# Performance work log

Measured on AMD Instinct MI355X. Metric: run time of the kernel, lower is better.

The kernel has to match this reference:

```python
import jax, jax.numpy as jnp
import numpy as np

H = 256

def setup_inputs() -> dict:
    key = jax.random.key(0)
    ks = jax.random.split(key, 9)
    s = 1.0 / np.sqrt(H)
    x = jax.random.normal(ks[0], (8, 2048, H), dtype=jnp.float32)
    Wq = jax.random.uniform(ks[1], (H, H), jnp.float32, -s, s)
    bq = jax.random.uniform(ks[2], (H,), jnp.float32, -s, s)
    Wk = jax.random.uniform(ks[3], (H, H), jnp.float32, -s, s)
    bk = jax.random.uniform(ks[4], (H,), jnp.float32, -s, s)
    Wv = jax.random.uniform(ks[5], (H, H), jnp.float32, -s, s)
    bv = jax.random.uniform(ks[6], (H,), jnp.float32, -s, s)
    Ww = jax.random.uniform(ks[7], (H, 1), jnp.float32, -s, s)
    bw = jax.random.uniform(ks[8], (1,), jnp.float32, -s, s)
    return {"x": x, "Wq": Wq, "bq": bq, "Wk": Wk, "bk": bk,
            "Wv": Wv, "bv": bv, "Ww": Ww, "bw": bw}

def reference(x, Wq, bq, Wk, bk, Wv, bv, Ww, bw):
    # x: (B, N, H) — cross-asset attention over N assets
    q = x @ Wq + bq
    k = x @ Wk + bk
    v = x @ Wv + bv
    scale = 1.0 / jnp.sqrt(jnp.asarray(q.shape[-1], q.dtype))
    beta = jnp.einsum('bnd,bmd->bnm', q, k) * scale  # (B, N, N)
    beta = jax.nn.softmax(beta, axis=-1)
    # original: sum(value[:,None] * beta[...,None], dim=2) == beta @ v
    out = jnp.einsum('bnm,bmd->bnd', beta, v)
    final_scores = (out @ Ww + bw)[..., 0]  # (B, N)
    return final_scores
```

## Files before the change

### kernel.cpp

```cpp
#include <hip/hip_runtime.h>

#define H 256
#define NB 2048
#define BATCH 8
#define NSPLIT 8
#define KSPAN (NB / NSPLIT)
#define NITER (KSPAN / 64)

typedef unsigned short u16;
using bf16x8 = __attribute__((ext_vector_type(8))) __bf16;
using f32x4  = __attribute__((ext_vector_type(4))) float;

typedef const __attribute__((address_space(1))) void gv_t;
typedef __attribute__((address_space(3))) void lv_t;

__device__ __forceinline__ void gl_lds16(const void* g, void* l) {
    __builtin_amdgcn_global_load_lds((gv_t*)g, (lv_t*)l, 16, 0, 0);
}

#define MFMA(a, b, c) __builtin_amdgcn_mfma_f32_16x16x32_bf16(a, b, c, 0, 0, 0)

__device__ __forceinline__ u16 f2bf(float f) {
    union { float f; unsigned u; } v; v.f = f;
    unsigned r = v.u + 0x7fffu + ((v.u >> 16) & 1u);
    return (u16)(r >> 16);
}

__global__ __launch_bounds__(256) void wprep_kernel(
        const float* __restrict__ Wq, const float* __restrict__ Wk,
        const float* __restrict__ Wv, const float* __restrict__ Ww,
        const float* __restrict__ bq,
        u16* __restrict__ wqb, u16* __restrict__ wkb,
        float* __restrict__ wvw, float* __restrict__ kbv) {
    int f = blockIdx.x, t = threadIdx.x;
    float wq = Wq[f * H + t];
    wqb[f * H + t] = f2bf(wq);
    float wk = Wk[f * H + t];
    wkb[f * H + t] = f2bf(wk);
    float p = Wv[f * H + t] * Ww[t];
    float r = wk * bq[t];
    for (int o = 32; o; o >>= 1) { p += __shfl_xor(p, o); r += __shfl_xor(r, o); }
    __shared__ float redp[4], redr[4];
    int w = t >> 6, lane = t & 63;
    if (lane == 0) { redp[w] = p; redr[w] = r; }
    __syncthreads();
    if (t == 0) {
        wvw[f] = redp[0] + redp[1] + redp[2] + redp[3];
        kbv[f] = redr[0] + redr[1] + redr[2] + redr[3];
    }
}

__global__ __launch_bounds__(256) void cvtu_kernel(
        const float* __restrict__ x, const float* __restrict__ wvw,
        const float* __restrict__ kbv, const float* __restrict__ bv,
        const float* __restrict__ Ww,
        u16* __restrict__ xbf, float2* __restrict__ uee) {
    int lane = threadIdx.x & 63;
    int row  = blockIdx.x * 4 + (threadIdx.x >> 6);
    float4 xv = *(const float4*)(x + row * H + lane * 4);
    ushort4 o;
    o.x = f2bf(xv.x); o.y = f2bf(xv.y); o.z = f2bf(xv.z); o.w = f2bf(xv.w);
    *(ushort4*)(xbf + row * H + lane * 4) = o;
    float4 wv = *(const float4*)(wvw + lane * 4);
    float s = xv.x * wv.x + xv.y * wv.y + xv.z * wv.z + xv.w * wv.w;
    float4 kv = *(const float4*)(kbv + lane * 4);
    float d = xv.x * kv.x + xv.y * kv.y + xv.z * kv.z + xv.w * kv.w;
    float4 bvv = *(const float4*)(bv + lane * 4);
    float4 www = *(const float4*)(Ww + lane * 4);
    float c = bvv.x * www.x + bvv.y * www.y + bvv.z * www.z + bvv.w * www.w;
    for (int o2 = 32; o2; o2 >>= 1) {
        s += __shfl_xor(s, o2); d += __shfl_xor(d, o2); c += __shfl_xor(c, o2);
    }
    if (lane == 0) {
        float e = __expf(d * 0.0625f);
        uee[row] = make_float2(e * (s + c), e);
    }
}

__global__ __launch_bounds__(256) void gemm_bt_kernel(
        const u16* __restrict__ A, const u16* __restrict__ B,
        u16* __restrict__ C, float scale) {
    __shared__ u16 bt[16384];
    int tid = threadIdx.x;
    int mb = blockIdx.x * 128, nb = blockIdx.y * 64;
    int w = tid >> 6, lane = tid & 63;
    int l15 = lane & 15, quad = lane >> 4;

    {
        const u16* gsrc = B + (nb + w * 16 + l15) * H + quad * 8;
        for (int ks = 0; ks < 8; ++ks)
            gl_lds16(gsrc + ks * 32, bt + (w * 8 + ks) * 512);
    }

    bf16x8 a[2][8];
    for (int mi = 0; mi < 2; ++mi) {
        const u16* abase = A + (size_t)(mb + w * 32 + mi * 16 + l15) * H + quad * 8;
        for (int ks = 0; ks < 8; ++ks) a[mi][ks] = *(const bf16x8*)(abase + ks * 32);
    }
    __syncthreads();

    f32x4 acc[2][4] = {};
    for (int ks = 0; ks < 8; ++ks)
        for (int t = 0; t < 4; ++t) {
            bf16x8 b = *(const bf16x8*)(bt + ((t * 8 + ks) * 64 + lane) * 8);
            acc[0][t] = MFMA(a[0][ks], b, acc[0][t]);
            acc[1][t] = MFMA(a[1][ks], b, acc[1][t]);
        }

    for (int mi = 0; mi < 2; ++mi) {
        int m = mb + w * 32 + mi * 16 + quad * 4;
        for (int t = 0; t < 4; ++t) {
            int n = nb + t * 16 + l15;
            for (int r = 0; r < 4; ++r)
                C[(size_t)(m + r) * H + n] = f2bf(acc[mi][t][r] * scale);
        }
    }
}

__global__ __launch_bounds__(256, 2) void attn_kernel(
        const u16* __restrict__ T, const u16* __restrict__ xbf,
        const float2* __restrict__ uee,
        float* __restrict__ pnum, float* __restrict__ pden) {
    __shared__ u16 kt[32768];
    int tid = threadIdx.x;
    int id = blockIdx.x;
    int b = id & 7, rest = id >> 3;
    int qc = rest & 7, sp = rest >> 3;
    int w = tid >> 6, lane = tid & 63, l15 = lane & 15, quad = lane >> 4;
    int qb = qc * 256;

    bf16x8 aq[4][8];
    {
        const u16* qbase = T + (size_t)(b * NB + qb + w * 64 + l15) * H + quad * 8;
        #pragma unroll
        for (int mi = 0; mi < 4; ++mi)
            #pragma unroll
            for (int ks = 0; ks < 8; ++ks)
                aq[mi][ks] = *(const bf16x8*)(qbase + mi * 16 * H + ks * 32);
    }

    const u16* xb = xbf + (size_t)b * NB * H;
    const float2* uep = uee + (size_t)b * NB;
    const int kb0 = sp * KSPAN;

    const u16* gsrc = xb + (size_t)(kb0 + w * 16 + l15) * H + quad * 8;
    #pragma unroll
    for (int j = 0; j < 8; ++j)
        gl_lds16(gsrc + j * 32, kt + (w * 8 + j) * 512);
    __syncthreads();

    float ls[4][4] = {}, as_[4][4] = {};

    #pragma unroll 1
    for (int h = 0; h < NITER; ++h) {
        const u16* ktc = kt + (h & 1) * 16384;
        if (h + 1 < NITER) {
            u16* dst = kt + ((h & 1) ^ 1) * 16384;
            const u16* g2 = gsrc + (size_t)(h + 1) * 64 * H;
            #pragma unroll
            for (int j = 0; j < 8; ++j)
                gl_lds16(g2 + j * 32, dst + (w * 8 + j) * 512);
        }
        int kb64 = kb0 + h * 64;
        float2 uv[4];
        #pragma unroll
        for (int t = 0; t < 4; ++t) uv[t] = uep[kb64 + t * 16 + l15];

        #pragma unroll
        for (int t = 0; t < 4; ++t) {
            f32x4 acc[4] = {};
            #pragma unroll
            for (int ks = 0; ks < 8; ++ks) {
                bf16x8 bfr = *(const bf16x8*)(ktc + ((t * 8 + ks) * 64 + lane) * 8);
                acc[0] = MFMA(aq[0][ks], bfr, acc[0]);
                acc[1] = MFMA(aq[1][ks], bfr, acc[1]);
                acc[2] = MFMA(aq[2][ks], bfr, acc[2]);
                acc[3] = MFMA(aq[3][ks], bfr, acc[3]);
            }
            #pragma unroll
            for (int mi = 0; mi < 4; ++mi)
                #pragma unroll
                for (int r = 0; r < 4; ++r) {
                    float p = __expf(acc[mi][r]);
                    as_[mi][r] += p * uv[t].x;
                    ls[mi][r]  += p * uv[t].y;
                }
        }
        __syncthreads();
    }

    #pragma unroll
    for (int mi = 0; mi < 4; ++mi)
        #pragma unroll
        for (int r = 0; r < 4; ++r)
            for (int o = 1; o < 16; o <<= 1) {
                ls[mi][r]  += __shfl_xor(ls[mi][r], o);
                as_[mi][r] += __shfl_xor(as_[mi][r], o);
            }

    if (l15 == 0) {
        size_t base = (size_t)(sp * BATCH + b) * NB + qb + w * 64 + quad * 4;
        #pragma unroll
        for (int mi = 0; mi < 4; ++mi)
            #pragma unroll
            for (int r = 0; r < 4; ++r) {
                pnum[base + mi * 16 + r] = as_[mi][r];
                pden[base + mi * 16 + r] = ls[mi][r];
            }
    }
}

__global__ __launch_bounds__(256) void finalize_kernel(
        const float* __restrict__ pnum, const float* __restrict__ pden,
        const float* __restrict__ bw, float* __restrict__ out) {
    int i = blockIdx.x * 256 + threadIdx.x;
    float num = 0.f, den = 0.f;
    for (int sp = 0; sp < NSPLIT; ++sp) {
        num += pnum[sp * (BATCH * NB) + i];
        den += pden[sp * (BATCH * NB) + i];
    }
    out[i] = num / den + bw[0];
}

extern "C" void kernel_launch(void* const* d_in, const int* in_sizes, int n_in,
                              void* d_out, int out_size, void* d_ws, size_t ws_size,
                              hipStream_t stream) {
    (void)in_sizes; (void)n_in; (void)out_size; (void)ws_size;
    const float* x  = (const float*)d_in[0];
    const float* Wq = (const float*)d_in[1];
    const float* bq = (const float*)d_in[2];
    const float* Wk = (const float*)d_in[3];
    const float* bk = (const float*)d_in[4];  (void)bk;
    const float* Wv = (const float*)d_in[5];
    const float* bv = (const float*)d_in[6];
    const float* Ww = (const float*)d_in[7];
    const float* bw = (const float*)d_in[8];
    float* out = (float*)d_out;

    u16* xbf = (u16*)d_ws;
    u16* Tbf = xbf + 4194304;
    u16* aTb = Tbf + 4194304;
    u16* wqb = aTb + 65536;
    u16* wkb = wqb + 65536;
    float* wvw = (float*)(wkb + 65536);
    float* kbv = wvw + 256;
    float2* uee = (float2*)(kbv + 256);
    float* pnum = (float*)(uee + 16384);
    float* pden = pnum + NSPLIT * BATCH * NB;

    hipLaunchKernelGGL(wprep_kernel, dim3(256), dim3(256), 0, stream,
                       Wq, Wk, Wv, Ww, bq, wqb, wkb, wvw, kbv);
    hipLaunchKernelGGL(gemm_bt_kernel, dim3(2, 4), dim3(256), 0, stream,
                       wkb, wqb, aTb, 0.0625f);
    hipLaunchKernelGGL(cvtu_kernel, dim3(4096), dim3(256), 0, stream,
                       x, wvw, kbv, bv, Ww, xbf, uee);
    hipLaunchKernelGGL(gemm_bt_kernel, dim3(128, 4), dim3(256), 0, stream,
                       xbf, aTb, Tbf, 1.0f);
    hipLaunchKernelGGL(attn_kernel, dim3(8 * 8 * NSPLIT), dim3(256), 0, stream,
                       Tbf, xbf, uee, pnum, pden);
    hipLaunchKernelGGL(finalize_kernel, dim3(64), dim3(256), 0, stream,
                       pnum, pden, bw, out);
}
```

Baseline: 126.8 us.

## Fuse weight prep with Wk·Wqᵀ GEMM and x conversion with projection GEMM

The prep pass now does the small Wk·Wqᵀ GEMM in the same launch as the bias/weight reductions, converting fp32 to bf16 on the fly so the separate weight-conversion buffers go away. The x-to-bf16 conversion and the per-row u/e reductions move into the x·aT GEMM, which reads x in fp32 directly. Only one of the four column-tile blocks writes xbf and uee. This cuts the launch count from six to four and drops a full read and write of x in bf16. The cost is that each x tile is read and converted four times in fp32. The attention MFMA loop also gains s_setprio hints to favour waves issuing matrix ops.

```diff
diff --git a/kernel.cpp b/kernel.cpp
--- a/kernel.cpp
+++ b/kernel.cpp
@@ -26,93 +26,173 @@
     return (u16)(r >> 16);
 }
 
-__global__ __launch_bounds__(256) void wprep_kernel(
+__device__ __forceinline__ bf16x8 cvt8(const float* p) {
+    float4 f0 = *(const float4*)p;
+    float4 f1 = *(const float4*)(p + 4);
+    union { bf16x8 v; u16 u[8]; } r;
+    r.u[0] = f2bf(f0.x); r.u[1] = f2bf(f0.y); r.u[2] = f2bf(f0.z); r.u[3] = f2bf(f0.w);
+    r.u[4] = f2bf(f1.x); r.u[5] = f2bf(f1.y); r.u[6] = f2bf(f1.z); r.u[7] = f2bf(f1.w);
+    return r.v;
+}
+
+__global__ __launch_bounds__(256) void prep_kernel(
         const float* __restrict__ Wq, const float* __restrict__ Wk,
         const float* __restrict__ Wv, const float* __restrict__ Ww,
-        const float* __restrict__ bq,
-        u16* __restrict__ wqb, u16* __restrict__ wkb,
-        float* __restrict__ wvw, float* __restrict__ kbv) {
-    int f = blockIdx.x, t = threadIdx.x;
-    float wq = Wq[f * H + t];
-    wqb[f * H + t] = f2bf(wq);
-    float wk = Wk[f * H + t];
-    wkb[f * H + t] = f2bf(wk);
-    float p = Wv[f * H + t] * Ww[t];
-    float r = wk * bq[t];
-    for (int o = 32; o; o >>= 1) { p += __shfl_xor(p, o); r += __shfl_xor(r, o); }
-    __shared__ float redp[4], redr[4];
-    int w = t >> 6, lane = t & 63;
-    if (lane == 0) { redp[w] = p; redr[w] = r; }
+        const float* __restrict__ bq, const float* __restrict__ bv,
+        u16* __restrict__ aTb, float* __restrict__ wvw,
+        float* __restrict__ kbv, float* __restrict__ ccp) {
+    __shared__ u16 bt[16384];
+    int id = blockIdx.x, t = threadIdx.x;
+
+    if (id < 256) {
+        int f = id;
+        float p = Wv[f * H + t] * Ww[t];
+        float r = Wk[f * H + t] * bq[t];
+        float c = (id == 0) ? bv[t] * Ww[t] : 0.f;
+        for (int o = 32; o; o >>= 1) {
+            p += __shfl_xor(p, o); r += __shfl_xor(r, o); c += __shfl_xor(c, o);
+        }
+        __shared__ float redp[4], redr[4], redc[4];
+        int w = t >> 6, lane = t & 63;
+        if (lane == 0) { redp[w] = p; redr[w] = r; redc[w] = c; }
+        __syncthreads();
+        if (t == 0) {
+            wvw[f] = redp[0] + redp[1] + redp[2] + redp[3];
+            kbv[f] = redr[0] + redr[1] + redr[2] + redr[3];
+            if (f == 0) ccp[0] = redc[0] + redc[1] + redc[2] + redc[3];
+        }
+        return;
+    }
+
+    int gid = id - 256;
+    int mb = (gid >> 2) * 128, nb = (gid & 3) * 64;
+    int w = t >> 6, lane = t & 63, l15 = lane & 15, quad = lane >> 4;
+
+    {
+        const float* src = Wq + (nb + w * 16 + l15) * H + quad * 8;
+        #pragma unroll
+        for (int ks = 0; ks < 8; ++ks)
+            *(bf16x8*)(bt + (w * 8 + ks) * 512 + lane * 8) = cvt8(src + ks * 32);
+    }
+
+    bf16x8 a[2][8];
+    #pragma unroll
+    for (int mi = 0; mi < 2; ++mi) {
+        const float* ab = Wk + (mb + w * 32 + mi * 16 + l15) * H + quad * 8;
+        #pragma unroll
+        for (int ks = 0; ks < 8; ++ks) a[mi][ks] = cvt8(ab + ks * 32);
+    }
     __syncthreads();
-    if (t == 0) {
-        wvw[f] = redp[0] + redp[1] + redp[2] + redp[3];
-        kbv[f] = redr[0] + redr[1] + redr[2] + redr[3];
-    }
-}
-
-__global__ __launch_bounds__(256) void cvtu_kernel(
-        const float* __restrict__ x, const float* __restrict__ wvw,
-        const float* __restrict__ kbv, const float* __restrict__ bv,
-        const float* __restrict__ Ww,
-        u16* __restrict__ xbf, float2* __restrict__ uee) {
-    int lane = threadIdx.x & 63;
-    int row  = blockIdx.x * 4 + (threadIdx.x >> 6);
-    float4 xv = *(const float4*)(x + row * H + lane * 4);
-    ushort4 o;
-    o.x = f2bf(xv.x); o.y = f2bf(xv.y); o.z = f2bf(xv.z); o.w = f2bf(xv.w);
-    *(ushort4*)(xbf + row * H + lane * 4) = o;
-    float4 wv = *(const float4*)(wvw + lane * 4);
-    float s = xv.x * wv.x + xv.y * wv.y + xv.z * wv.z + xv.w * wv.w;
-    float4 kv = *(const float4*)(kbv + lane * 4);
-    float d = xv.x * kv.x + xv.y * kv.y + xv.z * kv.z + xv.w * kv.w;
-    float4 bvv = *(const float4*)(bv + lane * 4);
-    float4 www = *(const float4*)(Ww + lane * 4);
-    float c = bvv.x * www.x + bvv.y * www.y + bvv.z * www.z + bvv.w * www.w;
-    for (int o2 = 32; o2; o2 >>= 1) {
-        s += __shfl_xor(s, o2); d += __shfl_xor(d, o2); c += __shfl_xor(c, o2);
-    }
-    if (lane == 0) {
-        float e = __expf(d * 0.0625f);
-        uee[row] = make_float2(e * (s + c), e);
-    }
-}
-
-__global__ __launch_bounds__(256) void gemm_bt_kernel(
-        const u16* __restrict__ A, const u16* __restrict__ B,
-        u16* __restrict__ C, float scale) {
+
+    f32x4 acc[2][4] = {};
+    #pragma unroll
+    for (int ks = 0; ks < 8; ++ks)
+        #pragma unroll
+        for (int tt = 0; tt < 4; ++tt) {
+            bf16x8 b = *(const bf16x8*)(bt + ((tt * 8 + ks) * 64 + lane) * 8);
+            acc[0][tt] = MFMA(a[0][ks], b, acc[0][tt]);
+            acc[1][tt] = MFMA(a[1][ks], b, acc[1][tt]);
+        }
+
+    #pragma unroll
+    for (int mi = 0; mi < 2; ++mi) {
+        int m = mb + w * 32 + mi * 16 + quad * 4;
+        #pragma unroll
+        for (int tt = 0; tt < 4; ++tt) {
+            int n = nb + tt * 16 + l15;
+            #pragma unroll
+            for (int r2 = 0; r2 < 4; ++r2)
+                aTb[(m + r2) * H + n] = f2bf(acc[mi][tt][r2] * 0.0625f);
+        }
+    }
+}
+
+__global__ __launch_bounds__(256) void xt_kernel(
+        const float* __restrict__ x, const u16* __restrict__ aTb,
+        const float* __restrict__ wvw, const float* __restrict__ kbv,
+        const float* __restrict__ ccp,
+        u16* __restrict__ xbf, float2* __restrict__ uee, u16* __restrict__ Tbf) {
     __shared__ u16 bt[16384];
-    int tid = threadIdx.x;
-    int mb = blockIdx.x * 128, nb = blockIdx.y * 64;
-    int w = tid >> 6, lane = tid & 63;
-    int l15 = lane & 15, quad = lane >> 4;
+    int id = blockIdx.x, tid = threadIdx.x;
+    int nbI = (id >> 3) & 3;
+    int mb4 = (id & 7) + (id >> 5) * 8;
+    int mb = mb4 * 128, nb = nbI * 64;
+    int w = tid >> 6, lane = tid & 63, l15 = lane & 15, quad = lane >> 4;
 
     {
-        const u16* gsrc = B + (nb + w * 16 + l15) * H + quad * 8;
+        const u16* gsrc = aTb + (nb + w * 16 + l15) * H + quad * 8;
+        #pragma unroll
         for (int ks = 0; ks < 8; ++ks)
             gl_lds16(gsrc + ks * 32, bt + (w * 8 + ks) * 512);
     }
 
     bf16x8 a[2][8];
-    for (int mi = 0; mi < 2; ++mi) {
-        const u16* abase = A + (size_t)(mb + w * 32 + mi * 16 + l15) * H + quad * 8;
-        for (int ks = 0; ks < 8; ++ks) a[mi][ks] = *(const bf16x8*)(abase + ks * 32);
+    float s[2] = {0.f, 0.f}, d[2] = {0.f, 0.f};
+    #pragma unroll
+    for (int ks = 0; ks < 8; ++ks) {
+        const float* wp = wvw + ks * 32 + quad * 8;
+        const float* kp = kbv + ks * 32 + quad * 8;
+        float4 w0 = *(const float4*)wp, w1 = *(const float4*)(wp + 4);
+        float4 k0 = *(const float4*)kp, k1 = *(const float4*)(kp + 4);
+        #pragma unroll
+        for (int mi = 0; mi < 2; ++mi) {
+            const float* xr = x + (size_t)(mb + w * 32 + mi * 16 + l15) * H + ks * 32 + quad * 8;
+            float4 f0 = *(const float4*)xr;
+            float4 f1 = *(const float4*)(xr + 4);
+            union { bf16x8 v; u16 u[8]; } r;
+            r.u[0] = f2bf(f0.x); r.u[1] = f2bf(f0.y); r.u[2] = f2bf(f0.z); r.u[3] = f2bf(f0.w);
+            r.u[4] = f2bf(f1.x); r.u[5] = f2bf(f1.y); r.u[6] = f2bf(f1.z); r.u[7] = f2bf(f1.w);
+            a[mi][ks] = r.v;
+            s[mi] += f0.x * w0.x + f0.y * w0.y + f0.z * w0.z + f0.w * w0.w
+                   + f1.x * w1.x + f1.y * w1.y + f1.z * w1.z + f1.w * w1.w;
+            d[mi] += f0.x * k0.x + f0.y * k0.y + f0.z * k0.z + f0.w * k0.w
+                   + f1.x * k1.x + f1.y * k1.y + f1.z * k1.z + f1.w * k1.w;
+        }
+    }
+
+    if (nbI == 0) {
+        #pragma unroll
+        for (int mi = 0; mi < 2; ++mi) {
+            u16* xo = xbf + (size_t)(mb + w * 32 + mi * 16 + l15) * H + quad * 8;
+            #pragma unroll
+            for (int ks = 0; ks < 8; ++ks)
+                *(bf16x8*)(xo + ks * 32) = a[mi][ks];
+        }
+        float cc = ccp[0];
+        #pragma unroll
+        for (int mi = 0; mi < 2; ++mi) {
+            float ss = s[mi] + __shfl_xor(s[mi], 16);
+            ss += __shfl_xor(ss, 32);
+            float dd = d[mi] + __shfl_xor(d[mi], 16);
+            dd += __shfl_xor(dd, 32);
+            if (quad == 0) {
+                int row = mb + w * 32 + mi * 16 + l15;
+                float e = __expf(dd * 0.0625f);
+                uee[row] = make_float2(e * (ss + cc), e);
+            }
+        }
     }
     __syncthreads();
 
     f32x4 acc[2][4] = {};
+    #pragma unroll
     for (int ks = 0; ks < 8; ++ks)
-        for (int t = 0; t < 4; ++t) {
-            bf16x8 b = *(const bf16x8*)(bt + ((t * 8 + ks) * 64 + lane) * 8);
-            acc[0][t] = MFMA(a[0][ks], b, acc[0][t]);
-            acc[1][t] = MFMA(a[1][ks], b, acc[1][t]);
-        }
-
+        #pragma unroll
+        for (int tt = 0; tt < 4; ++tt) {
+            bf16x8 b = *(const bf16x8*)(bt + ((tt * 8 + ks) * 64 + lane) * 8);
+            acc[0][tt] = MFMA(a[0][ks], b, acc[0][tt]);
+            acc[1][tt] = MFMA(a[1][ks], b, acc[1][tt]);
+        }
+
+    #pragma unroll
     for (int mi = 0; mi < 2; ++mi) {
         int m = mb + w * 32 + mi * 16 + quad * 4;
-        for (int t = 0; t < 4; ++t) {
-            int n = nb + t * 16 + l15;
-            for (int r = 0; r < 4; ++r)
-                C[(size_t)(m + r) * H + n] = f2bf(acc[mi][t][r] * scale);
+        #pragma unroll
+        for (int tt = 0; tt < 4; ++tt) {
+            int n = nb + tt * 16 + l15;
+            #pragma unroll
+            for (int r2 = 0; r2 < 4; ++r2)
+                Tbf[(size_t)(m + r2) * H + n] = f2bf(acc[mi][tt][r2]);
         }
     }
 }
@@ -169,6 +249,7 @@
         #pragma unroll
         for (int t = 0; t < 4; ++t) {
             f32x4 acc[4] = {};
+            __builtin_amdgcn_s_setprio(1);
             #pragma unroll
             for (int ks = 0; ks < 8; ++ks) {
                 bf16x8 bfr = *(const bf16x8*)(ktc + ((t * 8 + ks) * 64 + lane) * 8);
@@ -177,6 +258,7 @@
                 acc[2] = MFMA(aq[2][ks], bfr, acc[2]);
                 acc[3] = MFMA(aq[3][ks], bfr, acc[3]);
             }
+            __builtin_amdgcn_s_setprio(0);
             #pragma unroll
             for (int mi = 0; mi < 4; ++mi)
                 #pragma unroll
@@ -240,22 +322,17 @@
     u16* xbf = (u16*)d_ws;
     u16* Tbf = xbf + 4194304;
     u16* aTb = Tbf + 4194304;
-    u16* wqb = aTb + 65536;
-    u16* wkb = wqb + 65536;
-    float* wvw = (float*)(wkb + 65536);
+    float* wvw = (float*)(aTb + 65536);
     float* kbv = wvw + 256;
-    float2* uee = (float2*)(kbv + 256);
+    float* ccp = kbv + 256;
+    float2* uee = (float2*)(ccp + 4);
     float* pnum = (float*)(uee + 16384);
     float* pden = pnum + NSPLIT * BATCH * NB;
 
-    hipLaunchKernelGGL(wprep_kernel, dim3(256), dim3(256), 0, stream,
-                       Wq, Wk, Wv, Ww, bq, wqb, wkb, wvw, kbv);
-    hipLaunchKernelGGL(gemm_bt_kernel, dim3(2, 4), dim3(256), 0, stream,
-                       wkb, wqb, aTb, 0.0625f);
-    hipLaunchKernelGGL(cvtu_kernel, dim3(4096), dim3(256), 0, stream,
-                       x, wvw, kbv, bv, Ww, xbf, uee);
-    hipLaunchKernelGGL(gemm_bt_kernel, dim3(128, 4), dim3(256), 0, stream,
-                       xbf, aTb, Tbf, 1.0f);
+    hipLaunchKernelGGL(prep_kernel, dim3(264), dim3(256), 0, stream,
+                       Wq, Wk, Wv, Ww, bq, bv, aTb, wvw, kbv, ccp);
+    hipLaunchKernelGGL(xt_kernel, dim3(512), dim3(256), 0, stream,
+                       x, aTb, wvw, kbv, ccp, xbf, uee, Tbf);
     hipLaunchKernelGGL(attn_kernel, dim3(8 * 8 * NSPLIT), dim3(256), 0, stream,
                        Tbf, xbf, uee, pnum, pden);
     hipLaunchKernelGGL(finalize_kernel, dim3(64), dim3(256), 0, stream,
```

New measurement: 133.1 us. +5.0%, slower.

## Load key tiles directly into registers with double-buffered prefetch instead of LDS

Applied to the files above, without the earlier changes.

The attention kernel stops staging key tiles through shared memory with global_load_lds and block barriers. Each wave now loads its own 16-key B fragments straight from global memory into registers, ping-ponging two register buffers so the next tile's load overlaps the current MFMA work. It also raises wave priority around the MFMA loop with s_setprio. This removes LDS traffic and __syncthreads, but each of the four waves re-reads the same key rows from global/L2, and the extra register buffers add pressure under launch_bounds(256,2).

```diff
diff --git a/kernel.cpp b/kernel.cpp
--- a/kernel.cpp
+++ b/kernel.cpp
@@ -5,7 +5,7 @@
 #define BATCH 8
 #define NSPLIT 8
 #define KSPAN (NB / NSPLIT)
-#define NITER (KSPAN / 64)
+#define NTG (KSPAN / 16)
 
 typedef unsigned short u16;
 using bf16x8 = __attribute__((ext_vector_type(8))) __bf16;
@@ -121,7 +121,6 @@
         const u16* __restrict__ T, const u16* __restrict__ xbf,
         const float2* __restrict__ uee,
         float* __restrict__ pnum, float* __restrict__ pden) {
-    __shared__ u16 kt[32768];
     int tid = threadIdx.x;
     int id = blockIdx.x;
     int b = id & 7, rest = id >> 3;
@@ -139,55 +138,49 @@
                 aq[mi][ks] = *(const bf16x8*)(qbase + mi * 16 * H + ks * 32);
     }
 
-    const u16* xb = xbf + (size_t)b * NB * H;
-    const float2* uep = uee + (size_t)b * NB;
-    const int kb0 = sp * KSPAN;
-
-    const u16* gsrc = xb + (size_t)(kb0 + w * 16 + l15) * H + quad * 8;
-    #pragma unroll
-    for (int j = 0; j < 8; ++j)
-        gl_lds16(gsrc + j * 32, kt + (w * 8 + j) * 512);
-    __syncthreads();
+    const u16* xb = xbf + (size_t)(b * NB + sp * KSPAN + l15) * H + quad * 8;
+    const float2* uep = uee + (size_t)b * NB + sp * KSPAN + l15;
 
     float ls[4][4] = {}, as_[4][4] = {};
 
+#define LOADT(BUF, UV, tg) {                                              \
+    const u16* bp = xb + (size_t)(tg) * 16 * H;                           \
+    _Pragma("unroll")                                                     \
+    for (int ks = 0; ks < 8; ++ks) BUF[ks] = *(const bf16x8*)(bp + ks * 32); \
+    UV = uep[(tg) * 16]; }
+
+#define COMPUTE(BUF, UV) {                                                \
+    f32x4 acc[4] = {};                                                    \
+    __builtin_amdgcn_s_setprio(1);                                        \
+    _Pragma("unroll")                                                     \
+    for (int ks = 0; ks < 8; ++ks) {                                      \
+        acc[0] = MFMA(aq[0][ks], BUF[ks], acc[0]);                        \
+        acc[1] = MFMA(aq[1][ks], BUF[ks], acc[1]);                        \
+        acc[2] = MFMA(aq[2][ks], BUF[ks], acc[2]);                        \
+        acc[3] = MFMA(aq[3][ks], BUF[ks], acc[3]);                        \
+    }                                                                     \
+    __builtin_amdgcn_s_setprio(0);                                        \
+    _Pragma("unroll")                                                     \
+    for (int mi = 0; mi < 4; ++mi)                                        \
+        _Pragma("unroll")                                                 \
+        for (int r = 0; r < 4; ++r) {                                     \
+            float p = __expf(acc[mi][r]);                                 \
+            as_[mi][r] += p * UV.x;                                       \
+            ls[mi][r]  += p * UV.y;                                       \
+        } }
+
+    bf16x8 bufA[8], bufB[8];
+    float2 uvA, uvB;
+    LOADT(bufA, uvA, 0);
     #pragma unroll 1
-    for (int h = 0; h < NITER; ++h) {
-        const u16* ktc = kt + (h & 1) * 16384;
-        if (h + 1 < NITER) {
-            u16* dst = kt + ((h & 1) ^ 1) * 16384;
-            const u16* g2 = gsrc + (size_t)(h + 1) * 64 * H;
-            #pragma unroll
-            for (int j = 0; j < 8; ++j)
-                gl_lds16(g2 + j * 32, dst + (w * 8 + j) * 512);
-        }
-        int kb64 = kb0 + h * 64;
-        float2 uv[4];
-        #pragma unroll
-        for (int t = 0; t < 4; ++t) uv[t] = uep[kb64 + t * 16 + l15];
-
-        #pragma unroll
-        for (int t = 0; t < 4; ++t) {
-            f32x4 acc[4] = {};
-            #pragma unroll
-            for (int ks = 0; ks < 8; ++ks) {
-                bf16x8 bfr = *(const bf16x8*)(ktc + ((t * 8 + ks) * 64 + lane) * 8);
-                acc[0] = MFMA(aq[0][ks], bfr, acc[0]);
-                acc[1] = MFMA(aq[1][ks], bfr, acc[1]);
-                acc[2] = MFMA(aq[2][ks], bfr, acc[2]);
-                acc[3] = MFMA(aq[3][ks], bfr, acc[3]);
-            }
-            #pragma unroll
-            for (int mi = 0; mi < 4; ++mi)
-                #pragma unroll
-                for (int r = 0; r < 4; ++r) {
-                    float p = __expf(acc[mi][r]);
-                    as_[mi][r] += p * uv[t].x;
-                    ls[mi][r]  += p * uv[t].y;
-                }
-        }
-        __syncthreads();
-    }
+    for (int tg = 0; tg < NTG; tg += 2) {
+        LOADT(bufB, uvB, tg + 1);
+        COMPUTE(bufA, uvA);
+        if (tg + 2 < NTG) LOADT(bufA, uvA, tg + 2);
+        COMPUTE(bufB, uvB);
+    }
+#undef LOADT
+#undef COMPUTE
 
     #pragma unroll
     for (int mi = 0; mi < 4; ++mi)
```

Result: slower. 163.8 us (+29.1%).
